# Performance work log

Measured on AMD Instinct MI355X. Metric: run time of the kernel, lower is better.

Reference implementation:

```python
import jax, jax.numpy as jnp
import numpy as np

K = 3          # kernel_size
PAD = 1        # padding
HEADS = 4
C = 128
K2 = K * K


def setup_inputs() -> dict:
    key = jax.random.key(0)
    k1, k2, k3, k4 = jax.random.split(key, 4)
    B, H, W = 4, 128, 128
    x = jax.random.normal(k1, (B, H, W, C), jnp.float32)
    w_qkv = jax.random.normal(k2, (K2 * K2 * HEADS, C), jnp.float32) * 0.02
    w_v = jax.random.normal(k3, (K2, C, C), jnp.float32) * np.sqrt(2.0 / (K2 * C))
    w_proj = jax.random.normal(k4, (C, C), jnp.float32) * 0.02
    return {"x": x, "w_qkv": w_qkv, "w_v": w_v, "w_proj": w_proj}


def _csa(x, w_qkv, w_v, w_proj):
    B, H, W, Cc = x.shape
    hd = Cc // HEADS
    scale = hd ** (-0.5)
    N = H * W
    # attention map: Linear(C -> k^4*heads); pool is identity for stride=1
    att = jnp.einsum('bhwc,oc->bhwo', x, w_qkv)                      # [B,H,W,81*heads]
    att = att.reshape(B, N, HEADS, K2, K2).transpose(0, 2, 1, 3, 4)  # [B,heads,N,k2,k2]
    att = jax.nn.softmax(att * scale, axis=-1)
    # unfold x into per-location 3x3 windows (patch index p = di*K + dj)
    xp = jnp.pad(x, ((0, 0), (PAD, PAD), (PAD, PAD), (0, 0)))
    patches = jnp.stack([xp[:, di:di + H, dj:dj + W, :]
                         for di in range(K) for dj in range(K)], axis=3)  # [B,H,W,k2,C]
    v = patches.reshape(B, N, K2, Cc)
    # grouped 1x1 conv == per-window-position CxC matmul
    v = jnp.einsum('pij,bnpj->bnpi', w_v, v)                          # [B,N,k2,C]
    v = v.reshape(B, N, K2, HEADS, hd).transpose(0, 3, 1, 2, 4)       # [B,heads,N,k2,hd]
    out = jnp.einsum('bhnpq,bhnqd->bhnpd', att, v)                    # [B,heads,N,k2,hd]
    # -> [B, C, k2, H, W] with channel index = head*hd + d (matches torch fold layout)
    out = out.transpose(0, 1, 4, 3, 2).reshape(B, Cc, K2, H, W)
    # fold: scatter-add overlapping patches back to (H, W)
    acc = jnp.zeros((B, Cc, H + 2 * PAD, W + 2 * PAD), x.dtype)
    p = 0
    for di in range(K):
        for dj in range(K):
            acc = acc.at[:, :, di:di + H, dj:dj + W].add(out[:, :, p])
            p += 1
    y = acc[:, :, PAD:PAD + H, PAD:PAD + W].transpose(0, 2, 3, 1)     # [B,H,W,C]
    return jnp.einsum('bhwc,oc->bhwo', y, w_proj)


def reference(x, w_qkv, w_v, w_proj):
    return _csa(x, w_qkv, w_v, w_proj)
```

## Files before the change

kernel.cpp:

```cpp
#include <hip/hip_runtime.h>


typedef short bf16x8 __attribute__((ext_vector_type(8)));
typedef float f32x4  __attribute__((ext_vector_type(4)));
typedef float v2f    __attribute__((ext_vector_type(2)));

#define SCALE 0.17677669529663687f

__device__ __forceinline__ unsigned short f2bf(float f) {
  unsigned u = __float_as_uint(f);
  u = (u + 0x7fffu + ((u >> 16) & 1u)) >> 16;
  return (unsigned short)u;
}
__device__ __forceinline__ float bf2f(unsigned short s) {
  return __uint_as_float(((unsigned)s) << 16);
}
__device__ __forceinline__ unsigned pk2bf(float lo, float hi) {
  unsigned a = __float_as_uint(lo) + 0x8000u;
  unsigned b = __float_as_uint(hi) + 0x8000u;
  return __builtin_amdgcn_perm(b, a, 0x07060302u);
}
__device__ __forceinline__ bf16x8 ld16(const unsigned short* p) {
  union { bf16x8 v; uint4 u; } r;
  r.u = *(const uint4*)p;
  return r.v;
}

__global__ __launch_bounds__(256) void cvt_kernel(const float* __restrict__ wq,
                                                  const float* __restrict__ wv,
                                                  const float* __restrict__ wp,
                                                  unsigned short* __restrict__ wqb,
                                                  unsigned short* __restrict__ wvb,
                                                  unsigned short* __restrict__ wpb) {
  long i = ((long)blockIdx.x * 256 + threadIdx.x) * 4;
  if (i >= 205312) return;
  const float* src; unsigned short* dst; long off;
  if (i < 41472)       { src = wq; dst = wqb; off = i; }
  else if (i < 188928) { src = wv; dst = wvb; off = i - 41472; }
  else                 { src = wp; dst = wpb; off = i - 188928; }
  float4 v = *(const float4*)(src + off);
  ushort4 o;
  o.x = f2bf(v.x); o.y = f2bf(v.y); o.z = f2bf(v.z); o.w = f2bf(v.w);
  *(ushort4*)(dst + off) = o;
}

__device__ __forceinline__ void softmax9(const float* L, unsigned short* attile,
                                         int row, int p) {
  float mx = L[0];
#pragma unroll
  for (int q = 1; q < 9; q++) mx = fmaxf(mx, L[q]);
  float e[9], s = 0.f;
#pragma unroll
  for (int q = 0; q < 9; q++) { e[q] = __expf((L[q] - mx) * SCALE); s += e[q]; }
  float inv = 1.f / s;
#pragma unroll
  for (int q = 0; q < 9; q++) attile[row * 90 + q * 10 + p] = f2bf(e[q] * inv);
}

__global__ __launch_bounds__(512, 4) void att_kernel(const float* __restrict__ x,
                                                     const unsigned short* __restrict__ wqb,
                                                     unsigned* __restrict__ attb) {
  __shared__ unsigned short A[64 * 136];
  __shared__ unsigned short Bl[96 * 136];
  __shared__ float lg[64][84];
  const int t = threadIdx.x;
  const long m0 = (long)blockIdx.x * 64;
#pragma unroll
  for (int k = 0; k < 4; k++) {
    int i = t + k * 512;
    int row = i >> 5, seg = i & 31;
    float4 v = *(const float4*)(x + (m0 + row) * 128 + seg * 4);
    *(uint2*)((unsigned*)A + row * 68 + seg * 2) =
        make_uint2(pk2bf(v.x, v.y), pk2bf(v.z, v.w));
  }
  const int w = t >> 6, lane = t & 63, qd = lane >> 4, l15 = lane & 15;
  const int rw = w & 3, th = w >> 2;
  const int sr0 = t / 9, sp0 = t - sr0 * 9;
  const int sr1 = (t + 512) / 9, sp1 = (t + 512) - sr1 * 9;
  int dsto[6], srco[6];
#pragma unroll
  for (int k = 0; k < 6; k++) {
    int i = t + k * 512;
    if (i < 2880) {
      int q = i / 320, rem = i - q * 320, n = rem / 5, j = rem - n * 5;
      dsto[k] = (int)(((size_t)(q * 4) * 65536 + m0 + n) * 5 + j);
      srco[k] = n * 45 + q * 5 + j;
    } else { dsto[k] = -1; srco[k] = 0; }
  }
  __syncthreads();
  bf16x8 af[4];
#pragma unroll
  for (int kk = 0; kk < 4; kk++)
    af[kk] = ld16(A + (rw * 16 + l15) * 136 + kk * 32 + qd * 8);

  unsigned short* attile = Bl;
  for (int h = 0; h < 4; h++) {
    __syncthreads();
#pragma unroll
    for (int k = 0; k < 3; k++) {
      int i = t + k * 512;
      if (i < 1296) {
        int row = i >> 4, seg = i & 15;
        const uint4 v = *(const uint4*)(wqb + (long)(h * 81 + row) * 128 + seg * 8);
        *(uint4*)((unsigned*)Bl + row * 68 + seg * 4) = v;
      }
    }
    __syncthreads();
    f32x4 acc[3] = {};
#pragma unroll
    for (int kk = 0; kk < 4; kk++)
#pragma unroll
      for (int tn = 0; tn < 3; tn++) {
        bf16x8 bf = ld16(Bl + ((th * 3 + tn) * 16 + l15) * 136 + kk * 32 + qd * 8);
        acc[tn] = __builtin_amdgcn_mfma_f32_16x16x32_bf16(af[kk], bf, acc[tn], 0, 0, 0);
      }
#pragma unroll
    for (int tn = 0; tn < 3; tn++)
#pragma unroll
      for (int r = 0; r < 4; r++) {
        int col = (th * 3 + tn) * 16 + l15;
        if (col < 81) lg[rw * 16 + qd * 4 + r][col] = acc[tn][r];
      }
    __syncthreads();
    softmax9(&lg[sr0][sp0 * 9], attile, sr0, sp0);
    if (t < 64) softmax9(&lg[sr1][sp1 * 9], attile, sr1, sp1);
    __syncthreads();
#pragma unroll
    for (int k = 0; k < 6; k++)
      if (dsto[k] >= 0)
        attb[dsto[k] + h * 327680] = ((const unsigned*)attile)[srco[k]];
  }
}

__global__ __launch_bounds__(512, 4) void av_kernel(const float* __restrict__ x,
                                                    const unsigned short* __restrict__ wvb,
                                                    const unsigned* __restrict__ attb,
                                                    const unsigned short* __restrict__ wpb,
                                                    float* __restrict__ out) {
  __shared__ unsigned short A[144 * 136];
  __shared__ unsigned short S[100 * 136];
  __shared__ unsigned aLs[2400];
  const int t = threadIdx.x;
  const int bb = blockIdx.z;
  const int r0 = blockIdx.y * 8, c0 = blockIdx.x * 8;
  const int l15 = t & 15, qd = (t >> 4) & 3, wvi = t >> 6;
  const int n = (wvi & 3) * 16 + l15, lr = n >> 3, lc = n & 7;
  const int g = (wvi >> 2) * 4 + qd, head = g >> 1;
  const long nb = (long)bb * 16384;
  unsigned* Sdw = (unsigned*)S;
  unsigned* Adw = (unsigned*)A;

  int xbase_[7];
#pragma unroll
  for (int nt = 0; nt < 7; nt++) {
    int ml = nt * 16 + l15;
    xbase_[nt] = (ml / 10) * 12 + (ml % 10) + 13;
  }

#pragma unroll
  for (int k = 0; k < 9; k++) {
    int i = t + k * 512;
    int row = i >> 5, seg = i & 31;
    int gr = r0 - 2 + row / 12, gc = c0 - 2 + row % 12;
    float4 v = make_float4(0.f, 0.f, 0.f, 0.f);
    if (gr >= 0 && gr < 128 && gc >= 0 && gc < 128)
      v = *(const float4*)(x + (nb + gr * 128 + gc) * 128 + seg * 4);
    *(uint2*)(Adw + row * 68 + seg * 2) = make_uint2(pk2bf(v.x, v.y), pk2bf(v.z, v.w));
  }

  int aoff[4], aidx[4];
#pragma unroll
  for (int k = 0; k < 4; k++) {
    int i = t + k * 512;
    if (i < 2000) {
      int hh = i / 500, rem = i - hh * 500, row = rem / 5, j5 = rem - row * 5;
      int gr = r0 - 1 + row / 10, gc = c0 - 1 + row % 10;
      aidx[k] = hh * 600 + row * 6 + j5;
      aoff[k] = (gr >= 0 && gr < 128 && gc >= 0 && gc < 128)
                    ? (int)(((size_t)hh * 65536 + nb + gr * 128 + gc) * 5 + j5)
                    : -1;
    } else { aidx[k] = -1; aoff[k] = -1; }
  }
  const unsigned short* pwv = wvb + (size_t)(wvi * 16 + l15) * 128 + qd * 8;

  v2f y2[8];
#pragma unroll
  for (int i = 0; i < 8; i++) y2[i] = (v2f){0.f, 0.f};

  unsigned avv[4];
  bf16x8 wvf[4];

#define LOAD_A(qq)                                                              \
  { _Pragma("unroll") for (int k = 0; k < 4; k++)                               \
      avv[k] = (aoff[k] >= 0) ? attb[aoff[k] + (qq) * 1310720] : 0u; }
#define LOAD_WV(qq)                                                             \
  { _Pragma("unroll") for (int kk = 0; kk < 4; kk++)                            \
      wvf[kk] = *(const bf16x8*)(pwv + (size_t)(qq) * 16384 + kk * 32); }

  LOAD_A(0)
  LOAD_WV(0)

  for (int q = 0; q < 9; q++) {
    const int qoff = (q / 3) * 12 + (q % 3) - 13;
    __syncthreads();

#pragma unroll
    for (int k = 0; k < 4; k++)
      if (aidx[k] >= 0) aLs[aidx[k]] = avv[k];

    f32x4 acc[7];
#pragma unroll
    for (int nt = 0; nt < 7; nt++) acc[nt] = (f32x4){0.f, 0.f, 0.f, 0.f};
#pragma unroll
    for (int nt = 0; nt < 7; nt++) {
      int xr = xbase_[nt] + qoff;
      xr = xr > 143 ? 143 : xr;
      bf16x8 bx[4];
#pragma unroll
      for (int kk = 0; kk < 4; kk++)
        bx[kk] = ld16(A + xr * 136 + kk * 32 + qd * 8);
#pragma unroll
      for (int kk = 0; kk < 4; kk++)
        acc[nt] = __builtin_amdgcn_mfma_f32_16x16x32_bf16(wvf[kk], bx[kk],
                                                          acc[nt], 0, 0, 0);
    }
#pragma unroll
    for (int nt = 0; nt < 7; nt++) {
      int loc = nt * 16 + l15;
      if (loc < 100)
        *(uint2*)(Sdw + loc * 68 + wvi * 8 + qd * 2) =
            make_uint2(pk2bf(acc[nt][0], acc[nt][1]),
                       pk2bf(acc[nt][2], acc[nt][3]));
    }
    __syncthreads();
    if (q < 8) { LOAD_A(q + 1) LOAD_WV(q + 1) }

    const unsigned short* aS = (const unsigned short*)aLs;
    const int mlb = lr * 10 + lc + 11;
#pragma unroll
    for (int p = 0; p < 9; p++) {
      const int ml = mlb + (1 - p / 3) * 10 + (1 - p % 3);
      const float a = bf2f(aS[head * 1200 + ml * 12 + p]);
      const v2f a2 = {a, a};
      const uint4* Sr = (const uint4*)(Sdw + ml * 68 + g * 8);
#pragma unroll
      for (int v4 = 0; v4 < 2; v4++) {
        const uint4 u = Sr[v4];
        v2f xv;
        const int yi = v4 * 4;
        xv.x = __uint_as_float(u.x << 16); xv.y = __uint_as_float(u.x & 0xffff0000u);
        y2[yi + 0] += a2 * xv;
        xv.x = __uint_as_float(u.y << 16); xv.y = __uint_as_float(u.y & 0xffff0000u);
        y2[yi + 1] += a2 * xv;
        xv.x = __uint_as_float(u.z << 16); xv.y = __uint_as_float(u.z & 0xffff0000u);
        y2[yi + 2] += a2 * xv;
        xv.x = __uint_as_float(u.w << 16); xv.y = __uint_as_float(u.w & 0xffff0000u);
        y2[yi + 3] += a2 * xv;
      }
    }
  }

  __syncthreads();
  unsigned short* yb = A;
  {
    uint4 pk[2];
#pragma unroll
    for (int v4 = 0; v4 < 2; v4++) {
      pk[v4].x = pk2bf(y2[v4 * 4 + 0].x, y2[v4 * 4 + 0].y);
      pk[v4].y = pk2bf(y2[v4 * 4 + 1].x, y2[v4 * 4 + 1].y);
      pk[v4].z = pk2bf(y2[v4 * 4 + 2].x, y2[v4 * 4 + 2].y);
      pk[v4].w = pk2bf(y2[v4 * 4 + 3].x, y2[v4 * 4 + 3].y);
    }
    uint4* dst = (uint4*)(Adw + n * 68 + g * 8);
    dst[0] = pk[0]; dst[1] = pk[1];
  }
  __syncthreads();
  f32x4 pacc[4] = {};
#pragma unroll
  for (int kk = 0; kk < 4; kk++) {
    bf16x8 afr = ld16(yb + ((wvi & 3) * 16 + l15) * 136 + kk * 32 + qd * 8);
#pragma unroll
    for (int tn = 0; tn < 4; tn++) {
      bf16x8 bfr = *(const bf16x8*)(wpb + (((wvi >> 2) * 4 + tn) * 16 + l15) * 128 +
                                    kk * 32 + qd * 8);
      pacc[tn] = __builtin_amdgcn_mfma_f32_16x16x32_bf16(afr, bfr, pacc[tn], 0, 0, 0);
    }
  }
#pragma unroll
  for (int tn = 0; tn < 4; tn++)
#pragma unroll
    for (int r = 0; r < 4; r++) {
      int nl = (wvi & 3) * 16 + qd * 4 + r;
      int col = ((wvi >> 2) * 4 + tn) * 16 + l15;
      out[(nb + (r0 + (nl >> 3)) * 128 + (c0 + (nl & 7))) * 128 + col] = pacc[tn][r];
    }
}

extern "C" void kernel_launch(void* const* d_in, const int* in_sizes, int n_in,
                              void* d_out, int out_size, void* d_ws, size_t ws_size,
                              hipStream_t stream) {
  const float* x  = (const float*)d_in[0];
  const float* wq = (const float*)d_in[1];
  const float* wv = (const float*)d_in[2];
  const float* wp = (const float*)d_in[3];
  char* w = (char*)d_ws;
  unsigned*       attb = (unsigned*)w;
  unsigned short* wqb  = (unsigned short*)(w + 47185920);
  unsigned short* wvb  = wqb + 41472;
  unsigned short* wpb  = wvb + 147456;

  cvt_kernel<<<201, 256, 0, stream>>>(wq, wv, wp, wqb, wvb, wpb);
  att_kernel<<<1024, 512, 0, stream>>>(x, wqb, attb);
  dim3 g3(16, 16, 4);
  av_kernel<<<g3, 512, 0, stream>>>(x, wvb, attb, wpb, (float*)d_out);
}
```

Measured before the change: 205.5 us.

## Switch value-projection GEMM to 32x32x16 MFMA tiles with redistributed wave work

```diff
diff --git a/kernel.cpp b/kernel.cpp
--- a/kernel.cpp
+++ b/kernel.cpp
@@ -3,6 +3,7 @@
 
 typedef short bf16x8 __attribute__((ext_vector_type(8)));
 typedef float f32x4  __attribute__((ext_vector_type(4)));
+typedef float f32x16 __attribute__((ext_vector_type(16)));
 typedef float v2f    __attribute__((ext_vector_type(2)));
 
 #define SCALE 0.17677669529663687f
@@ -144,17 +145,19 @@
   const int bb = blockIdx.z;
   const int r0 = blockIdx.y * 8, c0 = blockIdx.x * 8;
   const int l15 = t & 15, qd = (t >> 4) & 3, wvi = t >> 6;
+  const int lane = t & 63, l31 = lane & 31, lh = lane >> 5;
+  const int mt = wvi & 3, np = wvi >> 2;
   const int n = (wvi & 3) * 16 + l15, lr = n >> 3, lc = n & 7;
   const int g = (wvi >> 2) * 4 + qd, head = g >> 1;
   const long nb = (long)bb * 16384;
   unsigned* Sdw = (unsigned*)S;
   unsigned* Adw = (unsigned*)A;
 
-  int xbase_[7];
-#pragma unroll
-  for (int nt = 0; nt < 7; nt++) {
-    int ml = nt * 16 + l15;
-    xbase_[nt] = (ml / 10) * 12 + (ml % 10) + 13;
+  int xb2[2];
+#pragma unroll
+  for (int i = 0; i < 2; i++) {
+    int ml = (np * 2 + i) * 32 + l31;
+    xb2[i] = (ml / 10) * 12 + (ml % 10) + 13;
   }
 
 #pragma unroll
@@ -181,21 +184,21 @@
                     : -1;
     } else { aidx[k] = -1; aoff[k] = -1; }
   }
-  const unsigned short* pwv = wvb + (size_t)(wvi * 16 + l15) * 128 + qd * 8;
+  const unsigned short* pwv = wvb + (size_t)(mt * 32 + l31) * 128 + lh * 8;
 
   v2f y2[8];
 #pragma unroll
   for (int i = 0; i < 8; i++) y2[i] = (v2f){0.f, 0.f};
 
   unsigned avv[4];
-  bf16x8 wvf[4];
+  bf16x8 wvf[8];
 
 #define LOAD_A(qq)                                                              \
   { _Pragma("unroll") for (int k = 0; k < 4; k++)                               \
       avv[k] = (aoff[k] >= 0) ? attb[aoff[k] + (qq) * 1310720] : 0u; }
 #define LOAD_WV(qq)                                                             \
-  { _Pragma("unroll") for (int kk = 0; kk < 4; kk++)                            \
-      wvf[kk] = *(const bf16x8*)(pwv + (size_t)(qq) * 16384 + kk * 32); }
+  { _Pragma("unroll") for (int ks = 0; ks < 8; ks++)                            \
+      wvf[ks] = *(const bf16x8*)(pwv + (size_t)(qq) * 16384 + ks * 16); }
 
   LOAD_A(0)
   LOAD_WV(0)
@@ -208,29 +211,26 @@
     for (int k = 0; k < 4; k++)
       if (aidx[k] >= 0) aLs[aidx[k]] = avv[k];
 
-    f32x4 acc[7];
-#pragma unroll
-    for (int nt = 0; nt < 7; nt++) acc[nt] = (f32x4){0.f, 0.f, 0.f, 0.f};
-#pragma unroll
-    for (int nt = 0; nt < 7; nt++) {
-      int xr = xbase_[nt] + qoff;
+#pragma unroll
+    for (int i = 0; i < 2; i++) {
+      int xr = xb2[i] + qoff;
       xr = xr > 143 ? 143 : xr;
-      bf16x8 bx[4];
-#pragma unroll
-      for (int kk = 0; kk < 4; kk++)
-        bx[kk] = ld16(A + xr * 136 + kk * 32 + qd * 8);
-#pragma unroll
-      for (int kk = 0; kk < 4; kk++)
-        acc[nt] = __builtin_amdgcn_mfma_f32_16x16x32_bf16(wvf[kk], bx[kk],
-                                                          acc[nt], 0, 0, 0);
-    }
-#pragma unroll
-    for (int nt = 0; nt < 7; nt++) {
-      int loc = nt * 16 + l15;
-      if (loc < 100)
-        *(uint2*)(Sdw + loc * 68 + wvi * 8 + qd * 2) =
-            make_uint2(pk2bf(acc[nt][0], acc[nt][1]),
-                       pk2bf(acc[nt][2], acc[nt][3]));
+      f32x16 acc;
+#pragma unroll
+      for (int r = 0; r < 16; r++) acc[r] = 0.f;
+#pragma unroll
+      for (int ks = 0; ks < 8; ks++) {
+        bf16x8 bx = ld16(A + xr * 136 + ks * 16 + lh * 8);
+        acc = __builtin_amdgcn_mfma_f32_32x32x16_bf16(wvf[ks], bx, acc, 0, 0, 0);
+      }
+      int loc = (np * 2 + i) * 32 + l31;
+      if (loc < 100) {
+#pragma unroll
+        for (int rg = 0; rg < 4; rg++)
+          *(uint2*)(Sdw + loc * 68 + mt * 16 + rg * 4 + lh * 2) =
+              make_uint2(pk2bf(acc[rg * 4 + 0], acc[rg * 4 + 1]),
+                         pk2bf(acc[rg * 4 + 2], acc[rg * 4 + 3]));
+      }
     }
     __syncthreads();
     if (q < 8) { LOAD_A(q + 1) LOAD_WV(q + 1) }
```

Measured after the change: 221.0 us. +7.6%, slower.

## Retile av_kernel v-projection MFMA to reuse B fragments; pre-swizzle weights

Applied to the files above, without the earlier changes.

```diff
diff --git a/kernel.cpp b/kernel.cpp
--- a/kernel.cpp
+++ b/kernel.cpp
@@ -30,18 +30,43 @@
                                                   const float* __restrict__ wv,
                                                   const float* __restrict__ wp,
                                                   unsigned short* __restrict__ wqb,
-                                                  unsigned short* __restrict__ wvb,
-                                                  unsigned short* __restrict__ wpb) {
-  long i = ((long)blockIdx.x * 256 + threadIdx.x) * 4;
-  if (i >= 205312) return;
-  const float* src; unsigned short* dst; long off;
-  if (i < 41472)       { src = wq; dst = wqb; off = i; }
-  else if (i < 188928) { src = wv; dst = wvb; off = i - 41472; }
-  else                 { src = wp; dst = wpb; off = i - 188928; }
-  float4 v = *(const float4*)(src + off);
-  ushort4 o;
-  o.x = f2bf(v.x); o.y = f2bf(v.y); o.z = f2bf(v.z); o.w = f2bf(v.w);
-  *(ushort4*)(dst + off) = o;
+                                                  unsigned short* __restrict__ wvb2,
+                                                  unsigned short* __restrict__ wpb2) {
+  int i = blockIdx.x * 256 + threadIdx.x;
+  if (i >= 30848) return;
+  if (i < 10368) {
+    long off = (long)i * 4;
+    float4 v = *(const float4*)(wq + off);
+    ushort4 o;
+    o.x = f2bf(v.x); o.y = f2bf(v.y); o.z = f2bf(v.z); o.w = f2bf(v.w);
+    *(ushort4*)(wqb + off) = o;
+    return;
+  }
+  const float* s;
+  unsigned short* d;
+  if (i < 28800) {
+    int it = i - 10368;
+    int l = it & 63, mk = it >> 6;
+    int kk = mk & 3, m = (mk >> 2) & 3, qcg = mk >> 4;
+    int cg = qcg & 1, q = qcg >> 1;
+    int chan = cg * 64 + m * 16 + (l & 15);
+    int k0 = kk * 32 + (l >> 4) * 8;
+    s = wv + (long)q * 16384 + chan * 128 + k0;
+    d = wvb2 + (long)it * 8;
+  } else {
+    int it = i - 28800;
+    int l = it & 63, kk = (it >> 6) & 3, tn = it >> 8;
+    int col = tn * 16 + (l & 15);
+    int k0 = kk * 32 + (l >> 4) * 8;
+    s = wp + (long)col * 128 + k0;
+    d = wpb2 + (long)it * 8;
+  }
+  float4 a = *(const float4*)s, b = *(const float4*)(s + 4);
+  ushort4 o0, o1;
+  o0.x = f2bf(a.x); o0.y = f2bf(a.y); o0.z = f2bf(a.z); o0.w = f2bf(a.w);
+  o1.x = f2bf(b.x); o1.y = f2bf(b.y); o1.z = f2bf(b.z); o1.w = f2bf(b.w);
+  *(ushort4*)d = o0;
+  *(ushort4*)(d + 4) = o1;
 }
 
 __device__ __forceinline__ void softmax9(const float* L, unsigned short* attile,
@@ -133,9 +158,9 @@
 }
 
 __global__ __launch_bounds__(512, 4) void av_kernel(const float* __restrict__ x,
-                                                    const unsigned short* __restrict__ wvb,
+                                                    const unsigned short* __restrict__ wvb2,
                                                     const unsigned* __restrict__ attb,
-                                                    const unsigned short* __restrict__ wpb,
+                                                    const unsigned short* __restrict__ wpb2,
                                                     float* __restrict__ out) {
   __shared__ unsigned short A[144 * 136];
   __shared__ unsigned short S[100 * 136];
@@ -144,17 +169,19 @@
   const int bb = blockIdx.z;
   const int r0 = blockIdx.y * 8, c0 = blockIdx.x * 8;
   const int l15 = t & 15, qd = (t >> 4) & 3, wvi = t >> 6;
+  const int lane = t & 63;
+  const int cg = wvi >> 2, lg = wvi & 3;
   const int n = (wvi & 3) * 16 + l15, lr = n >> 3, lc = n & 7;
   const int g = (wvi >> 2) * 4 + qd, head = g >> 1;
   const long nb = (long)bb * 16384;
   unsigned* Sdw = (unsigned*)S;
   unsigned* Adw = (unsigned*)A;
 
-  int xbase_[7];
-#pragma unroll
-  for (int nt = 0; nt < 7; nt++) {
-    int ml = nt * 16 + l15;
-    xbase_[nt] = (ml / 10) * 12 + (ml % 10) + 13;
+  int xbI[2];
+#pragma unroll
+  for (int i = 0; i < 2; i++) {
+    int ml = (lg * 2 + i) * 16 + l15;
+    xbI[i] = (ml / 10) * 12 + (ml % 10) + 13;
   }
 
 #pragma unroll
@@ -181,21 +208,23 @@
                     : -1;
     } else { aidx[k] = -1; aoff[k] = -1; }
   }
-  const unsigned short* pwv = wvb + (size_t)(wvi * 16 + l15) * 128 + qd * 8;
+  const unsigned short* pwv = wvb2 + cg * 8192 + lane * 8;
 
   v2f y2[8];
 #pragma unroll
   for (int i = 0; i < 8; i++) y2[i] = (v2f){0.f, 0.f};
 
   unsigned avv[4];
-  bf16x8 wvf[4];
+  bf16x8 wvf[4][4];
 
 #define LOAD_A(qq)                                                              \
   { _Pragma("unroll") for (int k = 0; k < 4; k++)                               \
       avv[k] = (aoff[k] >= 0) ? attb[aoff[k] + (qq) * 1310720] : 0u; }
 #define LOAD_WV(qq)                                                             \
-  { _Pragma("unroll") for (int kk = 0; kk < 4; kk++)                            \
-      wvf[kk] = *(const bf16x8*)(pwv + (size_t)(qq) * 16384 + kk * 32); }
+  { _Pragma("unroll") for (int m = 0; m < 4; m++)                               \
+    _Pragma("unroll") for (int kk = 0; kk < 4; kk++)                            \
+      wvf[m][kk] = *(const bf16x8*)(pwv + (size_t)(qq) * 16384 +                \
+                                    (m * 4 + kk) * 512); }
 
   LOAD_A(0)
   LOAD_WV(0)
@@ -208,29 +237,34 @@
     for (int k = 0; k < 4; k++)
       if (aidx[k] >= 0) aLs[aidx[k]] = avv[k];
 
-    f32x4 acc[7];
-#pragma unroll
-    for (int nt = 0; nt < 7; nt++) acc[nt] = (f32x4){0.f, 0.f, 0.f, 0.f};
-#pragma unroll
-    for (int nt = 0; nt < 7; nt++) {
-      int xr = xbase_[nt] + qoff;
-      xr = xr > 143 ? 143 : xr;
-      bf16x8 bx[4];
-#pragma unroll
-      for (int kk = 0; kk < 4; kk++)
-        bx[kk] = ld16(A + xr * 136 + kk * 32 + qd * 8);
-#pragma unroll
-      for (int kk = 0; kk < 4; kk++)
-        acc[nt] = __builtin_amdgcn_mfma_f32_16x16x32_bf16(wvf[kk], bx[kk],
-                                                          acc[nt], 0, 0, 0);
-    }
-#pragma unroll
-    for (int nt = 0; nt < 7; nt++) {
-      int loc = nt * 16 + l15;
-      if (loc < 100)
-        *(uint2*)(Sdw + loc * 68 + wvi * 8 + qd * 2) =
-            make_uint2(pk2bf(acc[nt][0], acc[nt][1]),
-                       pk2bf(acc[nt][2], acc[nt][3]));
+#pragma unroll
+    for (int i = 0; i < 2; i++) {
+      const int tile = lg * 2 + i;
+      if (tile * 16 < 100) {
+        int xr = xbI[i] + qoff;
+        xr = xr > 143 ? 143 : xr;
+        bf16x8 bx[4];
+#pragma unroll
+        for (int kk = 0; kk < 4; kk++)
+          bx[kk] = ld16(A + xr * 136 + kk * 32 + qd * 8);
+        f32x4 acc[4];
+#pragma unroll
+        for (int m = 0; m < 4; m++) acc[m] = (f32x4){0.f, 0.f, 0.f, 0.f};
+#pragma unroll
+        for (int kk = 0; kk < 4; kk++)
+#pragma unroll
+          for (int m = 0; m < 4; m++)
+            acc[m] = __builtin_amdgcn_mfma_f32_16x16x32_bf16(wvf[m][kk], bx[kk],
+                                                             acc[m], 0, 0, 0);
+        int loc = tile * 16 + l15;
+        if (loc < 100) {
+#pragma unroll
+          for (int m = 0; m < 4; m++)
+            *(uint2*)(Sdw + loc * 68 + cg * 32 + m * 8 + qd * 2) =
+                make_uint2(pk2bf(acc[m][0], acc[m][1]),
+                           pk2bf(acc[m][2], acc[m][3]));
+        }
+      }
     }
     __syncthreads();
     if (q < 8) { LOAD_A(q + 1) LOAD_WV(q + 1) }
@@ -281,8 +315,8 @@
     bf16x8 afr = ld16(yb + ((wvi & 3) * 16 + l15) * 136 + kk * 32 + qd * 8);
 #pragma unroll
     for (int tn = 0; tn < 4; tn++) {
-      bf16x8 bfr = *(const bf16x8*)(wpb + (((wvi >> 2) * 4 + tn) * 16 + l15) * 128 +
-                                    kk * 32 + qd * 8);
+      bf16x8 bfr = *(const bf16x8*)(wpb2 + (((wvi >> 2) * 4 + tn) * 4 + kk) * 512 +
+                                    lane * 8);
       pacc[tn] = __builtin_amdgcn_mfma_f32_16x16x32_bf16(afr, bfr, pacc[tn], 0, 0, 0);
     }
   }
@@ -306,11 +340,11 @@
   char* w = (char*)d_ws;
   unsigned*       attb = (unsigned*)w;
   unsigned short* wqb  = (unsigned short*)(w + 47185920);
-  unsigned short* wvb  = wqb + 41472;
-  unsigned short* wpb  = wvb + 147456;
-
-  cvt_kernel<<<201, 256, 0, stream>>>(wq, wv, wp, wqb, wvb, wpb);
+  unsigned short* wvb2 = wqb + 41472;
+  unsigned short* wpb2 = wvb2 + 147456;
+
+  cvt_kernel<<<121, 256, 0, stream>>>(wq, wv, wp, wqb, wvb2, wpb2);
   att_kernel<<<1024, 512, 0, stream>>>(x, wqb, attb);
   dim3 g3(16, 16, 4);
-  av_kernel<<<g3, 512, 0, stream>>>(x, wvb, attb, wpb, (float*)d_out);
-}
+  av_kernel<<<g3, 512, 0, stream>>>(x, wvb2, attb, wpb2, (float*)d_out);
+}
```

After: 247.0 us. +20.2%, slower.
